# Optimization experiments

Measured on AMD Instinct MI355X. Metric: run time of the kernel, lower is better.

## Reference

```python
import jax, jax.numpy as jnp
import numpy as np

L, H, DH, D, F, BLK, VOCAB = 2, 16, 128, 2048, 8192, 64, 32000
B, S, R = 16, 77, 16
LORA_SCALE = 32.0 / 16.0  # alpha / r

# standard bitsandbytes NF4 codebook
NF4 = jnp.array([-1.0, -0.6961928009986877, -0.5250730514526367,
                 -0.39491748809814453, -0.28444138169288635, -0.18477343022823334,
                 -0.09105003625154495, 0.0, 0.07958029955625534, 0.16093020141124725,
                 0.24611230194568634, 0.33791524171829224, 0.44070982933044434,
                 0.5626170039176941, 0.723855197429657, 1.0], dtype=jnp.float32)


def setup_inputs() -> dict:
    key = jax.random.key(0)
    ks = jax.random.split(key, 24)
    n = lambda k, sh, s=0.02: jax.random.normal(k, sh, jnp.float32) * s
    u = lambda k, sh: jax.random.uniform(k, sh, dtype=jnp.float32) * 0.02
    ri = lambda k, sh, hi: jax.random.randint(k, sh, 0, hi, jnp.int32)
    return {
        "input_ids": ri(ks[0], (B, S), VOCAB),
        "attention_mask": jnp.ones((B, S), jnp.int32),
        "embed": n(ks[1], (VOCAB, D)),
        "ln_attn": jnp.ones((L, D), jnp.float32),
        "ln_mlp": jnp.ones((L, D), jnp.float32),
        "ln_final": jnp.ones((D,), jnp.float32),
        "qkv_codes": ri(ks[2], (L, 3, D, D), 16),
        "qkv_absmax": u(ks[3], (L, 3, D, D // BLK)),
        "qkv_A": n(ks[4], (L, 3, R, D)),
        "qkv_B": n(ks[5], (L, 3, D, R), 0.01),
        "o_codes": ri(ks[6], (L, D, D), 16),
        "o_absmax": u(ks[7], (L, D, D // BLK)),
        "o_A": n(ks[8], (L, R, D)),
        "o_B": n(ks[9], (L, D, R), 0.01),
        "gu_codes": ri(ks[10], (L, 2, F, D), 16),
        "gu_absmax": u(ks[11], (L, 2, F, D // BLK)),
        "gu_A": n(ks[12], (L, 2, R, D)),
        "gu_B": n(ks[13], (L, 2, F, R), 0.01),
        "down_codes": ri(ks[14], (L, D, F), 16),
        "down_absmax": u(ks[15], (L, D, F // BLK)),
        "down_A": n(ks[16], (L, R, F)),
        "down_B": n(ks[17], (L, D, R), 0.01),
    }


def _rmsnorm(x, w, eps=1e-6):
    return x * jax.lax.rsqrt(jnp.mean(x * x, axis=-1, keepdims=True) + eps) * w


def _dequant(codes, absmax):
    # codes: (out, cin) ints in [0,16); absmax: (out, cin//BLK) blockwise scales
    out, cin = codes.shape
    w = NF4[codes].reshape(out, cin // BLK, BLK) * absmax[..., None]
    return w.reshape(out, cin)


def _qlora(x, codes, absmax, A, Bm):
    # NF4 dequant base matmul + rank-R LoRA delta (eval mode, no dropout)
    W = _dequant(codes, absmax)
    return x @ W.T + LORA_SCALE * ((x @ A.T) @ Bm.T)


def _rope_cache(seq):
    inv = 1.0 / (10000.0 ** (jnp.arange(0, DH, 2, dtype=jnp.float32) / DH))
    f = jnp.arange(seq, dtype=jnp.float32)[:, None] * inv  # (S, DH/2)
    emb = jnp.concatenate([f, f], axis=-1)                 # (S, DH)
    return jnp.cos(emb), jnp.sin(emb)


def _rope(x, cos, sin):
    # x: (B, H, S, DH), llama-style rotate_half
    x1, x2 = jnp.split(x, 2, axis=-1)
    return x * cos + jnp.concatenate([-x2, x1], axis=-1) * sin


def _forward(input_ids, attention_mask, embed, ln_attn, ln_mlp, ln_final,
             qkv_codes, qkv_absmax, qkv_A, qkv_B,
             o_codes, o_absmax, o_A, o_B,
             gu_codes, gu_absmax, gu_A, gu_B,
             down_codes, down_absmax, down_A, down_B):
    b, s = input_ids.shape
    h = embed[input_ids]                                    # (B, S, D)
    cos, sin = _rope_cache(s)
    pad = attention_mask.astype(bool)[:, None, None, :]     # (B,1,1,S)
    mask = pad & jnp.tril(jnp.ones((s, s), bool))
    inv_sqrt_dh = np.float32(1.0 / np.sqrt(DH))
    for l in range(L):
        x = _rmsnorm(h, ln_attn[l])
        q, k, v = [_qlora(x, qkv_codes[l, i], qkv_absmax[l, i], qkv_A[l, i], qkv_B[l, i])
                   .reshape(b, s, H, DH).transpose(0, 2, 1, 3) for i in range(3)]
        q, k = _rope(q, cos, sin), _rope(k, cos, sin)
        scores = jnp.einsum('bhqd,bhkd->bhqk', q, k) * inv_sqrt_dh
        attn = jax.nn.softmax(jnp.where(mask, scores, -1e9), axis=-1)
        o = jnp.einsum('bhqk,bhkd->bhqd', attn, v).transpose(0, 2, 1, 3).reshape(b, s, D)
        h = h + _qlora(o, o_codes[l], o_absmax[l], o_A[l], o_B[l])
        x = _rmsnorm(h, ln_mlp[l])
        g = _qlora(x, gu_codes[l, 0], gu_absmax[l, 0], gu_A[l, 0], gu_B[l, 0])
        up = _qlora(x, gu_codes[l, 1], gu_absmax[l, 1], gu_A[l, 1], gu_B[l, 1])
        h = h + _qlora(jax.nn.silu(g) * up,
                       down_codes[l], down_absmax[l], down_A[l], down_B[l])
    h = _rmsnorm(h, ln_final)
    lengths = attention_mask.sum(axis=1) - 1                # last non-pad token index
    return h[jnp.arange(b), lengths]                        # (B, D)


def reference(input_ids, attention_mask, embed, ln_attn, ln_mlp, ln_final,
              qkv_codes, qkv_absmax, qkv_A, qkv_B,
              o_codes, o_absmax, o_A, o_B,
              gu_codes, gu_absmax, gu_A, gu_B,
              down_codes, down_absmax, down_A, down_B):
    return _forward(input_ids, attention_mask, embed, ln_attn, ln_mlp, ln_final,
                    qkv_codes, qkv_absmax, qkv_A, qkv_B,
                    o_codes, o_absmax, o_A, o_B,
                    gu_codes, gu_absmax, gu_A, gu_B,
                    down_codes, down_absmax, down_A, down_B)
```

## Files before the change

kernel.cpp:

```cpp
#include <hip/hip_runtime.h>
#include <cstdint>
#include <cstddef>

#define M_TOK   1232
#define M_PAD   1280
#define D_MODEL 2048
#define F_FFN   8192
#define SEQ     77
#define BATCH   16
#define NHEAD   16
#define LRANK   16
#define NLAYER  2
#define ATILE   16

typedef short bf16x8 __attribute__((ext_vector_type(8)));
typedef float f32x4  __attribute__((ext_vector_type(4)));

__device__ __constant__ float NF4C[16] = {
  -1.0f, -0.6961928009986877f, -0.5250730514526367f, -0.39491748809814453f,
  -0.28444138169288635f, -0.18477343022823334f, -0.09105003625154495f, 0.0f,
  0.07958029955625534f, 0.16093020141124725f, 0.24611230194568634f,
  0.33791524171829224f, 0.44070982933044434f, 0.5626170039176941f,
  0.723855197429657f, 1.0f };

__device__ inline unsigned short f2b(float f) {
  unsigned u = __builtin_bit_cast(unsigned, f);
  u += 0x7FFFu + ((u >> 16) & 1u);
  return (unsigned short)(u >> 16);
}
__device__ inline float b2f(unsigned short s) {
  return __builtin_bit_cast(float, ((unsigned)s) << 16);
}

__global__ __launch_bounds__(256) void mat_w(
    const int* __restrict__ C, const float* __restrict__ AM,
    unsigned short* __restrict__ W, int K, long total8, int ilv)
{
  __shared__ float tb[16];
  if (threadIdx.x < 16) tb[threadIdx.x] = NF4C[threadIdx.x];
  __syncthreads();
  const int KB = K >> 6;
  for (long i = (long)blockIdx.x * 256 + threadIdx.x; i < total8;
       i += (long)gridDim.x * 256) {
    long e = i << 3;
    int rd = (int)(e / K), k = (int)(e - (long)rd * K);
    int srcn = ilv ? ((rd & 1) * F_FFN + (rd >> 1)) : rd;
    float am = AM[(size_t)srcn * KB + (k >> 6)];
    const int4* cp = (const int4*)(C + (size_t)srcn * K + k);
    int4 a = cp[0], b = cp[1];
    uint4 o;
    o.x = (unsigned)f2b(tb[a.x] * am) | ((unsigned)f2b(tb[a.y] * am) << 16);
    o.y = (unsigned)f2b(tb[a.z] * am) | ((unsigned)f2b(tb[a.w] * am) << 16);
    o.z = (unsigned)f2b(tb[b.x] * am) | ((unsigned)f2b(tb[b.y] * am) << 16);
    o.w = (unsigned)f2b(tb[b.z] * am) | ((unsigned)f2b(tb[b.w] * am) << 16);
    *(uint4*)(W + e) = o;
  }
}

__global__ __launch_bounds__(256, 2) void gemm_bf(
    const unsigned short* __restrict__ X, const unsigned short* __restrict__ W,
    float* __restrict__ O, int mb, int N, int K, int acc_mode, int splitk,
    const float* __restrict__ T, const float* __restrict__ Bm, int sh, int nr,
    int gum, unsigned short* __restrict__ GB)
{
  __shared__ __align__(16) unsigned short xs[128 * 64];
  __shared__ __align__(16) unsigned short ws[128 * 64];

  int tid = threadIdx.x;

  int nwg = gridDim.x;
  int q8 = nwg >> 3, r8 = nwg & 7;
  int xcd = blockIdx.x & 7, pos = blockIdx.x >> 3;
  int wgid = (xcd < r8) ? (xcd * (q8 + 1) + pos)
                        : (r8 * (q8 + 1) + (xcd - r8) * q8 + pos);
  int nb = N >> 7;
  int per = mb * nb;
  int slice = wgid / per; int rem = wgid - slice * per;
  int nblk = rem / mb, mblk = rem - nblk * mb;
  int row0 = mblk << 7, col0 = nblk << 7;
  int KBtot = K >> 6, kcnt = KBtot / splitk, kbeg = slice * kcnt;

  int wave = tid >> 6, lane = tid & 63;
  int fr = lane & 15, fg = lane >> 4, s7 = fr & 7;
  int wm = (wave >> 1) * 64, wn = (wave & 1) * 64;
  int xg = lane >> 3;
  int xcol = (((lane & 7) ^ (xg & 7)) << 3);

  const unsigned short* Xbase = X + (size_t)row0 * K + (size_t)kbeg * 64;
  const unsigned short* Wbase = W + (size_t)col0 * K + (size_t)kbeg * 64;

  f32x4 accm[4][4];
  #pragma unroll
  for (int i = 0; i < 4; ++i)
    #pragma unroll
    for (int j = 0; j < 4; ++j) accm[i][j] = (f32x4){0.f, 0.f, 0.f, 0.f};

  auto stage = [&](int t) {
    const unsigned short* xb = Xbase + (size_t)t * 64;
    const unsigned short* wb = Wbase + (size_t)t * 64;
    #pragma unroll
    for (int p2 = 0; p2 < 4; ++p2) {
      int c = wave * 4 + p2;
      const unsigned short* gp = xb + (size_t)(c * 8 + xg) * K + xcol;
      __builtin_amdgcn_global_load_lds(
          (const __attribute__((address_space(1))) unsigned int*)gp,
          (__attribute__((address_space(3))) unsigned int*)(xs + c * 512),
          16, 0, 0);
    }
    #pragma unroll
    for (int p2 = 0; p2 < 4; ++p2) {
      int c = wave * 4 + p2;
      const unsigned short* gp = wb + (size_t)(c * 8 + xg) * K + xcol;
      __builtin_amdgcn_global_load_lds(
          (const __attribute__((address_space(1))) unsigned int*)gp,
          (__attribute__((address_space(3))) unsigned int*)(ws + c * 512),
          16, 0, 0);
    }
  };
  auto compute = [&]() {
    bf16x8 b0[4], b1[4];
    #pragma unroll
    for (int ni = 0; ni < 4; ++ni) {
      const unsigned short* wr = ws + (wn + ni * 16 + fr) * 64;
      b0[ni] = *(const bf16x8*)(wr + ((fg ^ s7) << 3));
      b1[ni] = *(const bf16x8*)(wr + (((4 | fg) ^ s7) << 3));
    }
    #pragma unroll
    for (int mi = 0; mi < 4; ++mi) {
      const unsigned short* xr = xs + (wm + mi * 16 + fr) * 64;
      bf16x8 a0 = *(const bf16x8*)(xr + ((fg ^ s7) << 3));
      bf16x8 a1 = *(const bf16x8*)(xr + (((4 | fg) ^ s7) << 3));
      #pragma unroll
      for (int ni = 0; ni < 4; ++ni) {
        accm[mi][ni] = __builtin_amdgcn_mfma_f32_16x16x32_bf16(
            a0, b0[ni], accm[mi][ni], 0, 0, 0);
        accm[mi][ni] = __builtin_amdgcn_mfma_f32_16x16x32_bf16(
            a1, b1[ni], accm[mi][ni], 0, 0, 0);
      }
    }
  };

  stage(0);
  for (int t = 0; t < kcnt; ++t) {
    __syncthreads();
    compute();
    if (t + 1 < kcnt) {
      __syncthreads();
      stage(t + 1);
    }
  }

  if (gum) {
    float* Tt = (float*)&xs[0];
    float* Bt = (float*)&ws[0];
    __syncthreads();
    for (int idx = tid; idx < 128 * 32; idx += 256) {
      int rr = idx >> 5, c = idx & 31;
      int gm = row0 + rr;
      Tt[idx] = (gm < M_TOK) ? T[(size_t)gm * 32 + c] : 0.f;
    }
    for (int idx = tid; idx < 128 * 16; idx += 256) {
      int rr = idx >> 4, c = idx & 15;
      int type = rr & 1, nrow = (col0 + rr) >> 1;
      Bt[idx] = Bm[((size_t)type * F_FFN + nrow) * LRANK + c];
    }
    __syncthreads();
    #pragma unroll
    for (int mi = 0; mi < 4; ++mi)
      #pragma unroll
      for (int ni = 0; ni < 4; ++ni) {
        int gm0 = row0 + wm + mi * 16 + fg * 4;
        int gnl = wn + ni * 16 + fr;
        #pragma unroll
        for (int r = 0; r < 4; ++r) {
          int gm = gm0 + r;
          float vv = accm[mi][ni][r];
          const float* tr = Tt + (wm + mi * 16 + fg * 4 + r) * 32 + ((gnl & 1) << 4);
          const float* br = Bt + gnl * 16;
          float s = 0.f;
          #pragma unroll
          for (int c = 0; c < 16; ++c) s += tr[c] * br[c];
          vv += 2.0f * s;
          float prt = __shfl_xor(vv, 1);
          if (gm < M_TOK && !(fr & 1)) {
            float sig = 1.0f / (1.0f + expf(-vv));
            GB[(size_t)gm * F_FFN + ((col0 + gnl) >> 1)] = f2b(vv * sig * prt);
          }
        }
      }
    return;
  }

  float* Tt = (float*)&xs[0];
  float* Bt = (float*)&ws[0];
  if (T) {
    __syncthreads();
    int toff = (col0 >> sh) << 4;
    for (int idx = tid; idx < 128 * 16; idx += 256) {
      int rr = idx >> 4, c = idx & 15;
      int gm = row0 + rr;
      Tt[idx] = (gm < M_TOK) ? T[(size_t)gm * nr + toff + c] : 0.f;
      Bt[idx] = Bm[(size_t)(col0 + rr) * LRANK + c];
    }
    __syncthreads();
  }

  #pragma unroll
  for (int mi = 0; mi < 4; ++mi)
    #pragma unroll
    for (int ni = 0; ni < 4; ++ni) {
      int gm0 = row0 + wm + mi * 16 + fg * 4;
      int gnl = wn + ni * 16 + fr;
      int gn = col0 + gnl;
      #pragma unroll
      for (int r = 0; r < 4; ++r) {
        int gm = gm0 + r;
        if (gm < M_TOK) {
          size_t idx = (size_t)gm * N + gn;
          float vv = accm[mi][ni][r];
          if (T) {
            const float* tr = Tt + (wm + mi * 16 + fg * 4 + r) * 16;
            const float* br = Bt + gnl * 16;
            float s = 0.f;
            #pragma unroll
            for (int c = 0; c < 16; ++c) s += tr[c] * br[c];
            vv += 2.0f * s;
          }
          if (splitk > 1)       atomicAdd(&O[idx], vv);
          else if (acc_mode)    O[idx] += vv;
          else                  O[idx] = vv;
        }
      }
    }
}

__global__ __launch_bounds__(256) void lora1(
    const unsigned short* __restrict__ X, const float* __restrict__ A,
    float* __restrict__ T, int K)
{
  int m0 = blockIdx.x * 4, bi = blockIdx.y, nmat = gridDim.y;
  int g = threadIdx.x >> 4, l16 = threadIdx.x & 15;
  const float* ar = A + (size_t)bi * LRANK * K + (size_t)g * K;
  const unsigned short* x0 = X + (size_t)m0 * K;
  float s0 = 0.f, s1 = 0.f, s2 = 0.f, s3 = 0.f;
  for (int kk = l16 * 4; kk < K; kk += 64) {
    float4 av = *(const float4*)(ar + kk);
    ushort4 v0 = *(const ushort4*)(x0 + kk);
    ushort4 v1 = *(const ushort4*)(x0 + K + kk);
    ushort4 v2 = *(const ushort4*)(x0 + 2 * K + kk);
    ushort4 v3 = *(const ushort4*)(x0 + 3 * K + kk);
    s0 += b2f(v0.x)*av.x + b2f(v0.y)*av.y + b2f(v0.z)*av.z + b2f(v0.w)*av.w;
    s1 += b2f(v1.x)*av.x + b2f(v1.y)*av.y + b2f(v1.z)*av.z + b2f(v1.w)*av.w;
    s2 += b2f(v2.x)*av.x + b2f(v2.y)*av.y + b2f(v2.z)*av.z + b2f(v2.w)*av.w;
    s3 += b2f(v3.x)*av.x + b2f(v3.y)*av.y + b2f(v3.z)*av.z + b2f(v3.w)*av.w;
  }
  #pragma unroll
  for (int off = 8; off; off >>= 1) {
    s0 += __shfl_down(s0, off, 16);
    s1 += __shfl_down(s1, off, 16);
    s2 += __shfl_down(s2, off, 16);
    s3 += __shfl_down(s3, off, 16);
  }
  if (l16 == 0) {
    size_t base = ((size_t)m0 * nmat + bi) * LRANK + g;
    size_t rs = (size_t)nmat * LRANK;
    T[base] = s0; T[base + rs] = s1; T[base + 2*rs] = s2; T[base + 3*rs] = s3;
  }
}

__global__ __launch_bounds__(256) void lora2(
    float* __restrict__ O, const float* __restrict__ T,
    const float* __restrict__ Bm, int N, int sh, int nr)
{
  int m0 = blockIdx.y * 8;
  int n = blockIdx.x * 256 + threadIdx.x;
  __shared__ float ts[8 * 48];
  for (int i = threadIdx.x; i < 8 * nr; i += 256)
    ts[(i / nr) * 48 + (i % nr)] = T[(size_t)(m0 + i / nr) * nr + (i % nr)];
  __syncthreads();
  const float4* br = (const float4*)(Bm + (size_t)n * LRANK);
  float4 b0 = br[0], b1 = br[1], b2 = br[2], b3 = br[3];
  int toff = ((n >> sh) << 4);
  #pragma unroll
  for (int mi = 0; mi < 8; ++mi) {
    const float* tsb = ts + mi * 48 + toff;
    float s = b0.x*tsb[0] + b0.y*tsb[1] + b0.z*tsb[2] + b0.w*tsb[3]
            + b1.x*tsb[4] + b1.y*tsb[5] + b1.z*tsb[6] + b1.w*tsb[7]
            + b2.x*tsb[8] + b2.y*tsb[9] + b2.z*tsb[10] + b2.w*tsb[11]
            + b3.x*tsb[12] + b3.y*tsb[13] + b3.z*tsb[14] + b3.w*tsb[15];
    O[(size_t)(m0 + mi) * N + n] += 2.0f * s;
  }
}

__global__ __launch_bounds__(256) void rmsnorm_k(
    const float* __restrict__ H, const float* __restrict__ W,
    unsigned short* __restrict__ X, int D)
{
  int m = blockIdx.x;
  const float* hr = H + (size_t)m * D;
  float s = 0.f;
  for (int i = threadIdx.x; i < D; i += 256) { float v = hr[i]; s += v * v; }
  __shared__ float red[4];
  #pragma unroll
  for (int off = 32; off; off >>= 1) s += __shfl_down(s, off, 64);
  if ((threadIdx.x & 63) == 0) red[threadIdx.x >> 6] = s;
  __syncthreads();
  float tot = red[0] + red[1] + red[2] + red[3];
  float inv = rsqrtf(tot / (float)D + 1e-6f);
  for (int i = threadIdx.x; i < D; i += 256)
    X[(size_t)m * D + i] = f2b(hr[i] * inv * W[i]);
}

__global__ void rope_table(float* __restrict__ cosT, float* __restrict__ sinT)
{
  int idx = blockIdx.x * 64 + threadIdx.x;
  if (idx >= SEQ * 64) return;
  int s = idx >> 6, j = idx & 63;
  float inv = powf(10000.0f, -(float)(2 * j) / 128.0f);
  float f = (float)s * inv;
  cosT[idx] = cosf(f);
  sinT[idx] = sinf(f);
}

__global__ __launch_bounds__(256) void attn_k(
    const float* __restrict__ QKV, const int* __restrict__ amask,
    const float* __restrict__ cosT, const float* __restrict__ sinT,
    unsigned short* __restrict__ O)
{
  int bh = blockIdx.x, it = blockIdx.y;
  int b = bh >> 4, h = bh & (NHEAD - 1);
  const int STR = 3 * D_MODEL;
  __shared__ float ks[SEQ * 132];
  __shared__ float qs[ATILE * 132];
  __shared__ float sc[ATILE * 80];
  __shared__ int am[SEQ];
  const float scale = 0.08838834764831845f;

  const float* Kb = QKV + (size_t)(b * SEQ) * STR + D_MODEL + h * 128;
  for (int idx = threadIdx.x; idx < SEQ * 16; idx += 256) {
    int j = idx >> 4, dq = (idx & 15) << 2;
    float4 a = *(const float4*)(Kb + (size_t)j * STR + dq);
    float4 bb = *(const float4*)(Kb + (size_t)j * STR + dq + 64);
    float4 c4 = *(const float4*)(cosT + j * 64 + dq);
    float4 s4 = *(const float4*)(sinT + j * 64 + dq);
    float* kr = ks + j * 132 + dq;
    kr[0] = a.x*c4.x - bb.x*s4.x; kr[1] = a.y*c4.y - bb.y*s4.y;
    kr[2] = a.z*c4.z - bb.z*s4.z; kr[3] = a.w*c4.w - bb.w*s4.w;
    kr[64] = bb.x*c4.x + a.x*s4.x; kr[65] = bb.y*c4.y + a.y*s4.y;
    kr[66] = bb.z*c4.z + a.z*s4.z; kr[67] = bb.w*c4.w + a.w*s4.w;
  }
  const float* Qb = QKV + (size_t)(b * SEQ) * STR + h * 128;
  for (int idx = threadIdx.x; idx < ATILE * 16; idx += 256) {
    int il = idx >> 4, dq = (idx & 15) << 2;
    int i = it * ATILE + il;
    if (i < SEQ) {
      float4 a = *(const float4*)(Qb + (size_t)i * STR + dq);
      float4 bb = *(const float4*)(Qb + (size_t)i * STR + dq + 64);
      float4 c4 = *(const float4*)(cosT + i * 64 + dq);
      float4 s4 = *(const float4*)(sinT + i * 64 + dq);
      float* qr = qs + il * 132 + dq;
      qr[0] = a.x*c4.x - bb.x*s4.x; qr[1] = a.y*c4.y - bb.y*s4.y;
      qr[2] = a.z*c4.z - bb.z*s4.z; qr[3] = a.w*c4.w - bb.w*s4.w;
      qr[64] = bb.x*c4.x + a.x*s4.x; qr[65] = bb.y*c4.y + a.y*s4.y;
      qr[66] = bb.z*c4.z + a.z*s4.z; qr[67] = bb.w*c4.w + a.w*s4.w;
    }
  }
  for (int j = threadIdx.x; j < SEQ; j += 256) am[j] = amask[b * SEQ + j];
  __syncthreads();

  int wave = threadIdx.x >> 6, lane = threadIdx.x & 63;
  #pragma unroll
  for (int r = 0; r < 4; ++r) {
    int il = wave * 4 + r;
    int i = it * ATILE + il;
    if (i < SEQ) {
      const float4* qr = (const float4*)(qs + il * 132);
      int j1 = lane, j2 = lane + 64;
      float v1 = -1e9f, v2 = -1e9f;
      if (j1 <= i && am[j1]) {
        const float4* kr = (const float4*)(ks + j1 * 132);
        float s = 0.f;
        #pragma unroll 8
        for (int d = 0; d < 32; ++d) {
          float4 a = qr[d], c = kr[d];
          s += a.x*c.x + a.y*c.y + a.z*c.z + a.w*c.w;
        }
        v1 = s * scale;
      }
      if (j2 < SEQ && j2 <= i && am[j2]) {
        const float4* kr = (const float4*)(ks + j2 * 132);
        float s = 0.f;
        #pragma unroll 8
        for (int d = 0; d < 32; ++d) {
          float4 a = qr[d], c = kr[d];
          s += a.x*c.x + a.y*c.y + a.z*c.z + a.w*c.w;
        }
        v2 = s * scale;
      }
      float mx = fmaxf(v1, v2);
      #pragma unroll
      for (int off = 32; off; off >>= 1) mx = fmaxf(mx, __shfl_xor(mx, off));
      float e1 = __expf(v1 - mx);
      float e2 = (j2 < SEQ) ? __expf(v2 - mx) : 0.f;
      float sum = e1 + e2;
      #pragma unroll
      for (int off = 32; off; off >>= 1) sum += __shfl_xor(sum, off);
      float inv = 1.0f / sum;
      sc[il * 80 + j1] = e1 * inv;
      if (j2 < SEQ) sc[il * 80 + j2] = e2 * inv;
    }
  }
  __syncthreads();

  const float* Vbase = QKV + (size_t)(b * SEQ) * STR + 2 * D_MODEL + h * 128;
  for (int idx = threadIdx.x; idx < ATILE * 32; idx += 256) {
    int il = idx >> 5, d4 = (idx & 31) << 2;
    int i = it * ATILE + il;
    if (i >= SEQ) continue;
    float4 acc = {0.f, 0.f, 0.f, 0.f};
    const float* sr = sc + il * 80;
    for (int j = 0; j < SEQ; ++j) {
      float pp = sr[j];
      float4 v = *(const float4*)(Vbase + (size_t)j * STR + d4);
      acc.x += pp * v.x; acc.y += pp * v.y; acc.z += pp * v.z; acc.w += pp * v.w;
    }
    unsigned short* op = O + (size_t)(b * SEQ + i) * D_MODEL + h * 128 + d4;
    op[0] = f2b(acc.x); op[1] = f2b(acc.y); op[2] = f2b(acc.z); op[3] = f2b(acc.w);
  }
}

__global__ void embed_gather(const float* __restrict__ E, const int* __restrict__ ids,
                             float* __restrict__ H)
{
  size_t idx = (size_t)blockIdx.x * 256 + threadIdx.x;
  int m = (int)(idx / D_MODEL);
  int n = (int)(idx % D_MODEL);
  H[idx] = E[(size_t)ids[m] * D_MODEL + n];
}

__global__ __launch_bounds__(256) void final_k(
    const float* __restrict__ H, const int* __restrict__ amask,
    const float* __restrict__ W, float* __restrict__ out)
{
  int b = blockIdx.x;
  __shared__ int len;
  if (threadIdx.x == 0) {
    int s = 0;
    for (int j = 0; j < SEQ; ++j) s += amask[b * SEQ + j];
    len = s - 1;
  }
  __syncthreads();
  const float* hr = H + ((size_t)(b * SEQ + len) * D_MODEL);
  float s = 0.f;
  for (int i = threadIdx.x; i < D_MODEL; i += 256) { float v = hr[i]; s += v * v; }
  __shared__ float red[4];
  #pragma unroll
  for (int off = 32; off; off >>= 1) s += __shfl_down(s, off, 64);
  if ((threadIdx.x & 63) == 0) red[threadIdx.x >> 6] = s;
  __syncthreads();
  float tot = red[0] + red[1] + red[2] + red[3];
  float inv = rsqrtf(tot / (float)D_MODEL + 1e-6f);
  for (int i = threadIdx.x; i < D_MODEL; i += 256)
    out[(size_t)b * D_MODEL + i] = hr[i] * inv * W[i];
}

extern "C" void kernel_launch(void* const* d_in, const int* in_sizes, int n_in,
                              void* d_out, int out_size, void* d_ws, size_t ws_size,
                              hipStream_t stream) {
  const int*   ids     = (const int*)d_in[0];
  const int*   amask   = (const int*)d_in[1];
  const float* embed   = (const float*)d_in[2];
  const float* ln_attn = (const float*)d_in[3];
  const float* ln_mlp  = (const float*)d_in[4];
  const float* ln_fin  = (const float*)d_in[5];
  const int*   qkvC    = (const int*)d_in[6];
  const float* qkvS    = (const float*)d_in[7];
  const float* qkvA    = (const float*)d_in[8];
  const float* qkvB    = (const float*)d_in[9];
  const int*   oC      = (const int*)d_in[10];
  const float* oS      = (const float*)d_in[11];
  const float* oA      = (const float*)d_in[12];
  const float* oB      = (const float*)d_in[13];
  const int*   guC     = (const int*)d_in[14];
  const float* guS     = (const float*)d_in[15];
  const float* guA     = (const float*)d_in[16];
  const float* guB     = (const float*)d_in[17];
  const int*   dnC     = (const int*)d_in[18];
  const float* dnS     = (const float*)d_in[19];
  const float* dnA     = (const float*)d_in[20];
  const float* dnB     = (const float*)d_in[21];
  float* out = (float*)d_out;

  const int M = M_TOK, Mp = M_PAD, D = D_MODEL, F = F_FFN, R = LRANK;
  float* p = (float*)d_ws;
  float* h    = p; p += (size_t)Mp * D;
  float* qkv  = p; p += (size_t)Mp * 3 * D;
  float* t    = p; p += (size_t)Mp * 48;
  float* cosT = p; p += SEQ * 64;
  float* sinT = p; p += SEQ * 64;
  unsigned short* xbf = (unsigned short*)p; p += (size_t)Mp * D / 2;
  unsigned short* gbf = (unsigned short*)p; p += (size_t)Mp * F / 2;
  unsigned short* wbuf = (unsigned short*)p;
  p += (size_t)2 * F * D / 2;

  rope_table<<<(SEQ*64 + 63)/64, 64, 0, stream>>>(cosT, sinT);
  embed_gather<<<(M * D)/256, 256, 0, stream>>>(embed, ids, h);

  const int mb = Mp / 128;

  for (int l = 0; l < NLAYER; ++l) {
    rmsnorm_k<<<M, 256, 0, stream>>>(h, ln_attn + (size_t)l * D, xbf, D);
    lora1<<<dim3(M/4, 3), 256, 0, stream>>>(xbf, qkvA + (size_t)l*3*R*D, t, D);
    mat_w<<<4096, 256, 0, stream>>>(qkvC + (size_t)l*3*D*D, qkvS + (size_t)l*3*D*(D/64),
                                    wbuf, D, (long)3*D*D/8, 0);
    gemm_bf<<<mb * (3*D/128), 256, 0, stream>>>(
        xbf, wbuf, qkv, mb, 3*D, D, 0, 1,
        t, qkvB + (size_t)l*3*D*R, 11, 48, 0, nullptr);
    attn_k<<<dim3(BATCH*NHEAD, (SEQ + ATILE - 1)/ATILE), 256, 0, stream>>>(
        qkv, amask, cosT, sinT, xbf);
    mat_w<<<2048, 256, 0, stream>>>(oC + (size_t)l*D*D, oS + (size_t)l*D*(D/64),
                                    wbuf, D, (long)D*D/8, 0);
    gemm_bf<<<mb * (D/128) * 4, 256, 0, stream>>>(
        xbf, wbuf, h, mb, D, D, 1, 4, nullptr, nullptr, 0, 0, 0, nullptr);
    lora1<<<dim3(M/4, 1), 256, 0, stream>>>(xbf, oA + (size_t)l*R*D, t, D);
    lora2<<<dim3(D/256, M/8), 256, 0, stream>>>(h, t, oB + (size_t)l*D*R, D, 11, 16);

    rmsnorm_k<<<M, 256, 0, stream>>>(h, ln_mlp + (size_t)l * D, xbf, D);
    lora1<<<dim3(M/4, 2), 256, 0, stream>>>(xbf, guA + (size_t)l*2*R*D, t, D);
    mat_w<<<4096, 256, 0, stream>>>(guC + (size_t)l*2*F*D, guS + (size_t)l*2*F*(D/64),
                                    wbuf, D, (long)2*F*D/8, 1);
    gemm_bf<<<mb * (2*F/128), 256, 0, stream>>>(
        xbf, wbuf, nullptr, mb, 2*F, D, 0, 1,
        t, guB + (size_t)l*2*F*R, 0, 32, 1, gbf);
    mat_w<<<4096, 256, 0, stream>>>(dnC + (size_t)l*D*F, dnS + (size_t)l*D*(F/64),
                                    wbuf, F, (long)D*F/8, 0);
    gemm_bf<<<mb * (D/128) * 8, 256, 0, stream>>>(
        gbf, wbuf, h, mb, D, F, 1, 8, nullptr, nullptr, 0, 0, 0, nullptr);
    lora1<<<dim3(M/4, 1), 256, 0, stream>>>(gbf, dnA + (size_t)l*R*F, t, F);
    lora2<<<dim3(D/256, M/8), 256, 0, stream>>>(h, t, dnB + (size_t)l*D*R, D, 11, 16);
  }
  final_k<<<BATCH, 256, 0, stream>>>(h, amask, ln_fin, out);
}
```

Measured before the change: 1.234 ms.

## Overlap next weight dequantization with current GEMM via extra workgroups

Separate NF4 dequant launches are removed. Each GEMM launch now carries 512 extra workgroups that dequantize the weights needed by the next GEMM into their own dedicated buffers, so dequantization runs alongside the current GEMM rather than serialized before it. The first QKV dequant is issued up front. This uses more workspace (four weight buffers instead of one) and the GEMM and dequant work now compete for CUs and memory bandwidth inside one launch.

```diff
diff --git a/kernel.cpp b/kernel.cpp
--- a/kernel.cpp
+++ b/kernel.cpp
@@ -12,6 +12,7 @@
 #define LRANK   16
 #define NLAYER  2
 #define ATILE   16
+#define MWB     512
 
 typedef short bf16x8 __attribute__((ext_vector_type(8)));
 typedef float f32x4  __attribute__((ext_vector_type(4)));
@@ -61,14 +62,42 @@
     const unsigned short* __restrict__ X, const unsigned short* __restrict__ W,
     float* __restrict__ O, int mb, int N, int K, int acc_mode, int splitk,
     const float* __restrict__ T, const float* __restrict__ Bm, int sh, int nr,
-    int gum, unsigned short* __restrict__ GB)
+    int gum, unsigned short* __restrict__ GB,
+    const int* __restrict__ C2, const float* __restrict__ AM2,
+    unsigned short* __restrict__ W2, int K2, long total8_2, int ilv2, int Ggemm)
 {
   __shared__ __align__(16) unsigned short xs[128 * 64];
   __shared__ __align__(16) unsigned short ws[128 * 64];
 
   int tid = threadIdx.x;
 
-  int nwg = gridDim.x;
+  if ((int)blockIdx.x >= Ggemm) {
+    if (total8_2 > 0) {
+      float* tb = (float*)xs;
+      if (tid < 16) tb[tid] = NF4C[tid];
+      __syncthreads();
+      int nblk2 = gridDim.x - Ggemm;
+      const int KB2 = K2 >> 6;
+      for (long i = (long)((int)blockIdx.x - Ggemm) * 256 + tid; i < total8_2;
+           i += (long)nblk2 * 256) {
+        long e = i << 3;
+        int rd = (int)(e / K2), k = (int)(e - (long)rd * K2);
+        int srcn = ilv2 ? ((rd & 1) * F_FFN + (rd >> 1)) : rd;
+        float am = AM2[(size_t)srcn * KB2 + (k >> 6)];
+        const int4* cp = (const int4*)(C2 + (size_t)srcn * K2 + k);
+        int4 a = cp[0], b = cp[1];
+        uint4 o;
+        o.x = (unsigned)f2b(tb[a.x] * am) | ((unsigned)f2b(tb[a.y] * am) << 16);
+        o.y = (unsigned)f2b(tb[a.z] * am) | ((unsigned)f2b(tb[a.w] * am) << 16);
+        o.z = (unsigned)f2b(tb[b.x] * am) | ((unsigned)f2b(tb[b.y] * am) << 16);
+        o.w = (unsigned)f2b(tb[b.z] * am) | ((unsigned)f2b(tb[b.w] * am) << 16);
+        *(uint4*)(W2 + e) = o;
+      }
+    }
+    return;
+  }
+
+  int nwg = Ggemm;
   int q8 = nwg >> 3, r8 = nwg & 7;
   int xcd = blockIdx.x & 7, pos = blockIdx.x >> 3;
   int wgid = (xcd < r8) ? (xcd * (q8 + 1) + pos)
@@ -500,42 +529,52 @@
   float* sinT = p; p += SEQ * 64;
   unsigned short* xbf = (unsigned short*)p; p += (size_t)Mp * D / 2;
   unsigned short* gbf = (unsigned short*)p; p += (size_t)Mp * F / 2;
-  unsigned short* wbuf = (unsigned short*)p;
-  p += (size_t)2 * F * D / 2;
+  unsigned short* wQ = (unsigned short*)p; p += (size_t)3 * D * D / 2;
+  unsigned short* wO = (unsigned short*)p; p += (size_t)D * D / 2;
+  unsigned short* wG = (unsigned short*)p; p += (size_t)2 * F * D / 2;
+  unsigned short* wD = (unsigned short*)p; p += (size_t)D * F / 2;
 
   rope_table<<<(SEQ*64 + 63)/64, 64, 0, stream>>>(cosT, sinT);
   embed_gather<<<(M * D)/256, 256, 0, stream>>>(embed, ids, h);
+  mat_w<<<2048, 256, 0, stream>>>(qkvC, qkvS, wQ, D, (long)3*D*D/8, 0);
 
   const int mb = Mp / 128;
+  const int Gqkv = mb * (3*D/128);
+  const int Go   = mb * (D/128) * 4;
+  const int Ggu  = mb * (2*F/128);
+  const int Gdn  = mb * (D/128) * 8;
 
   for (int l = 0; l < NLAYER; ++l) {
     rmsnorm_k<<<M, 256, 0, stream>>>(h, ln_attn + (size_t)l * D, xbf, D);
     lora1<<<dim3(M/4, 3), 256, 0, stream>>>(xbf, qkvA + (size_t)l*3*R*D, t, D);
-    mat_w<<<4096, 256, 0, stream>>>(qkvC + (size_t)l*3*D*D, qkvS + (size_t)l*3*D*(D/64),
-                                    wbuf, D, (long)3*D*D/8, 0);
-    gemm_bf<<<mb * (3*D/128), 256, 0, stream>>>(
-        xbf, wbuf, qkv, mb, 3*D, D, 0, 1,
-        t, qkvB + (size_t)l*3*D*R, 11, 48, 0, nullptr);
+    gemm_bf<<<Gqkv + MWB, 256, 0, stream>>>(
+        xbf, wQ, qkv, mb, 3*D, D, 0, 1,
+        t, qkvB + (size_t)l*3*D*R, 11, 48, 0, nullptr,
+        oC + (size_t)l*D*D, oS + (size_t)l*D*(D/64), wO, D, (long)D*D/8, 0, Gqkv);
     attn_k<<<dim3(BATCH*NHEAD, (SEQ + ATILE - 1)/ATILE), 256, 0, stream>>>(
         qkv, amask, cosT, sinT, xbf);
-    mat_w<<<2048, 256, 0, stream>>>(oC + (size_t)l*D*D, oS + (size_t)l*D*(D/64),
-                                    wbuf, D, (long)D*D/8, 0);
-    gemm_bf<<<mb * (D/128) * 4, 256, 0, stream>>>(
-        xbf, wbuf, h, mb, D, D, 1, 4, nullptr, nullptr, 0, 0, 0, nullptr);
+    gemm_bf<<<Go + MWB, 256, 0, stream>>>(
+        xbf, wO, h, mb, D, D, 1, 4, nullptr, nullptr, 0, 0, 0, nullptr,
+        guC + (size_t)l*2*F*D, guS + (size_t)l*2*F*(D/64), wG, D, (long)2*F*D/8, 1, Go);
     lora1<<<dim3(M/4, 1), 256, 0, stream>>>(xbf, oA + (size_t)l*R*D, t, D);
     lora2<<<dim3(D/256, M/8), 256, 0, stream>>>(h, t, oB + (size_t)l*D*R, D, 11, 16);
 
     rmsnorm_k<<<M, 256, 0, stream>>>(h, ln_mlp + (size_t)l * D, xbf, D);
     lora1<<<dim3(M/4, 2), 256, 0, stream>>>(xbf, guA + (size_t)l*2*R*D, t, D);
-    mat_w<<<4096, 256, 0, stream>>>(guC + (size_t)l*2*F*D, guS + (size_t)l*2*F*(D/64),
-                                    wbuf, D, (long)2*F*D/8, 1);
-    gemm_bf<<<mb * (2*F/128), 256, 0, stream>>>(
-        xbf, wbuf, nullptr, mb, 2*F, D, 0, 1,
-        t, guB + (size_t)l*2*F*R, 0, 32, 1, gbf);
-    mat_w<<<4096, 256, 0, stream>>>(dnC + (size_t)l*D*F, dnS + (size_t)l*D*(F/64),
-                                    wbuf, F, (long)D*F/8, 0);
-    gemm_bf<<<mb * (D/128) * 8, 256, 0, stream>>>(
-        gbf, wbuf, h, mb, D, F, 1, 8, nullptr, nullptr, 0, 0, 0, nullptr);
+    gemm_bf<<<Ggu + MWB, 256, 0, stream>>>(
+        xbf, wG, nullptr, mb, 2*F, D, 0, 1,
+        t, guB + (size_t)l*2*F*R, 0, 32, 1, gbf,
+        dnC + (size_t)l*D*F, dnS + (size_t)l*D*(F/64), wD, F, (long)D*F/8, 0, Ggu);
+    if (l + 1 < NLAYER) {
+      gemm_bf<<<Gdn + MWB, 256, 0, stream>>>(
+          gbf, wD, h, mb, D, F, 1, 8, nullptr, nullptr, 0, 0, 0, nullptr,
+          qkvC + (size_t)(l+1)*3*D*D, qkvS + (size_t)(l+1)*3*D*(D/64),
+          wQ, D, (long)3*D*D/8, 0, Gdn);
+    } else {
+      gemm_bf<<<Gdn, 256, 0, stream>>>(
+          gbf, wD, h, mb, D, F, 1, 8, nullptr, nullptr, 0, 0, 0, nullptr,
+          nullptr, nullptr, nullptr, D, 0, 0, Gdn);
+    }
     lora1<<<dim3(M/4, 1), 256, 0, stream>>>(gbf, dnA + (size_t)l*R*F, t, F);
     lora2<<<dim3(D/256, M/8), 256, 0, stream>>>(h, t, dnB + (size_t)l*D*R, D, 11, 16);
   }
```

Result: faster. 1.192 ms (-3.4%).
